# Kernel optimization log

Hardware: AMD Instinct MI355X
Metric: run time of the kernel (lower is better)

Reference implementation:

```python
import jax, jax.numpy as jnp
import numpy as np

DIM = 192
HEADS = 6
WIN = 64  # 8*8
EPS = 1e-12


def setup_inputs() -> dict:
    key = jax.random.key(0)
    ks = jax.random.split(key, 10)
    s = 0.02
    return {
        "qx": jax.random.normal(ks[0], (8192, WIN, DIM), jnp.float32),
        "kvx": jax.random.normal(ks[1], (4096, WIN, DIM), jnp.float32),
        "pos": jax.random.normal(ks[2], (1, WIN, DIM), jnp.float32) * s,
        "Wq": jax.random.normal(ks[3], (DIM, DIM), jnp.float32) * s,
        "bq": jnp.zeros((DIM,), jnp.float32),
        "Wkv": jax.random.normal(ks[4], (2 * DIM, DIM), jnp.float32) * s,
        "bkv": jnp.zeros((2 * DIM,), jnp.float32),
        "Wp": jax.random.normal(ks[5], (DIM, DIM), jnp.float32) * s,
        "bp": jnp.zeros((DIM,), jnp.float32),
    }


def _l2norm(x):
    # F.normalize: x / max(||x||_2, eps) along last dim
    n = jnp.sqrt(jnp.sum(x * x, axis=-1, keepdims=True))
    return x / jnp.maximum(n, EPS)


def reference(qx, kvx, pos, Wq, bq, Wkv, bkv, Wp, bp):
    B_q, q_len, C = qx.shape
    B_kv, kv_len, _ = kvx.shape
    tile_num = B_q // B_kv
    kvx = jnp.tile(kvx, (tile_num, 1, 1))
    qx = qx + pos
    q = qx @ Wq.T + bq                       # [Bq, q, C]
    kv = kvx @ Wkv.T + bkv                   # [Bq, kv, 2C]
    k, v = kv[..., :C], kv[..., C:]
    hd = C // HEADS
    q = q.reshape(B_q, q_len, HEADS, hd).transpose(0, 2, 1, 3)
    k = k.reshape(B_q, kv_len, HEADS, hd).transpose(0, 2, 1, 3)
    v = v.reshape(B_q, kv_len, HEADS, hd).transpose(0, 2, 1, 3)
    scale = 1.0 / np.sqrt(C).astype(np.float32)
    attn = jnp.einsum("bhqd,bhkd->bhqk", _l2norm(q), _l2norm(k)) * scale
    attn = jax.nn.softmax(attn, axis=-1)
    x = jnp.einsum("bhqk,bhkd->bhqd", attn, v)
    x = x.transpose(0, 2, 1, 3).reshape(B_q, q_len, C)
    return x @ Wp.T + bp
```

## Files before the change

kernel.cpp:

```cpp
#include <hip/hip_runtime.h>
#include <hip/hip_bf16.h>

#define TPB   512
#define CDIM  192
#define LDA   200
#define LDST  200
#define SCALE 0.07216878364870323f
#define EPSF  1e-12f

using short8 = __attribute__((ext_vector_type(8))) short;
using f32x4  = __attribute__((ext_vector_type(4))) float;
using us4    = __attribute__((ext_vector_type(4))) unsigned short;

__device__ __forceinline__ unsigned short hc(float f) {
  __hip_bfloat16 h = __float2bfloat16(f);
  unsigned short u; __builtin_memcpy(&u, &h, 2); return u;
}
__device__ __forceinline__ unsigned pack2(float x, float y) {
  return (unsigned)hc(x) | ((unsigned)hc(y) << 16);
}
#define MFMA(a, b, c) __builtin_amdgcn_mfma_f32_16x16x32_bf16((a), (b), (c), 0, 0, 0)
#define SCHED_FENCE() __builtin_amdgcn_sched_barrier(0)

#define NWQ  36864
#define NWKV 73728
#define NWP  36864
__global__ void cvt_weights(const float* __restrict__ Wq, const float* __restrict__ Wkv,
                            const float* __restrict__ Wp, unsigned short* __restrict__ o) {
  int i = blockIdx.x * blockDim.x + threadIdx.x;
  if (i < NWQ) o[i] = hc(Wq[i]);
  else if (i < NWQ + NWKV) o[i] = hc(Wkv[i - NWQ]);
  else if (i < NWQ + NWKV + NWP) o[i] = hc(Wp[i - NWQ - NWKV]);
}

__global__ __launch_bounds__(TPB, 4) void wa_v13(
    const float* __restrict__ qx, const float* __restrict__ kvx,
    const float* __restrict__ pos,
    const float* __restrict__ bq, const float* __restrict__ bkv,
    const float* __restrict__ bp,
    const unsigned short* __restrict__ Wqb, const unsigned short* __restrict__ Wkvb,
    const unsigned short* __restrict__ Wpb,
    float* __restrict__ out, int BQ, int BKV)
{
  __shared__ __align__(16) unsigned short sA[64 * LDA];
  __shared__ __align__(16) unsigned short sU[64 * LDST];

  const int tid = threadIdx.x;
  const int wid = tid >> 6;
  const int l15 = (tid & 63) & 15;
  const int l4  = (tid & 63) >> 4;

  int g = blockIdx.x;
  int w;
  if (BQ == 2 * BKV && (BKV & 7) == 0) {
    w = ((g >> 4) << 3) + (g & 7) + (((g >> 3) & 1) ? BKV : 0);
  } else {
    w = g;
  }
  const size_t qoff  = (size_t)w * (64 * CDIM);
  const size_t kvoff = (size_t)(w % BKV) * (64 * CDIM);

  const int srcA = l15 + 32 * (l4 & 1);
  const int srcB = srcA + 16;
  const int sel  = l4 >> 1;
  auto redistC = [&](f32x4 cA, f32x4 cB) -> short8 {
    unsigned iA0 = pack2(cA[0], cA[1]), iA1 = pack2(cA[2], cA[3]);
    unsigned iB0 = pack2(cB[0], cB[1]), iB1 = pack2(cB[2], cB[3]);
    unsigned A00 = (unsigned)__shfl((int)iA0, srcA);
    unsigned A01 = (unsigned)__shfl((int)iA1, srcA);
    unsigned A10 = (unsigned)__shfl((int)iB0, srcA);
    unsigned A11 = (unsigned)__shfl((int)iB1, srcA);
    unsigned B00 = (unsigned)__shfl((int)iA0, srcB);
    unsigned B01 = (unsigned)__shfl((int)iA1, srcB);
    unsigned B10 = (unsigned)__shfl((int)iB0, srcB);
    unsigned B11 = (unsigned)__shfl((int)iB1, srcB);
    union { uint4 u; short8 s; } uu;
    uu.u.x = sel ? A10 : A00;
    uu.u.y = sel ? A11 : A01;
    uu.u.z = sel ? B10 : B00;
    uu.u.w = sel ? B11 : B01;
    return uu.s;
  };

  {
    const float4* gq = (const float4*)(qx + qoff);
    const float4* p4 = (const float4*)pos;
    #pragma unroll
    for (int t = 0; t < 6; ++t) {
      int e = tid + t * TPB, row = e / 48, c4 = e % 48;
      float4 a = gq[e], p = p4[e];
      us4 wq;
      wq.x = hc(a.x + p.x); wq.y = hc(a.y + p.y); wq.z = hc(a.z + p.z); wq.w = hc(a.w + p.w);
      *(us4*)&sA[row * LDA + c4 * 4] = wq;
    }
    const float4* gk = (const float4*)(kvx + kvoff);
    #pragma unroll
    for (int t = 0; t < 6; ++t) {
      int e = tid + t * TPB, row = e / 48, c4 = e % 48;
      float4 k = gk[e];
      us4 wk; wk.x = hc(k.x); wk.y = hc(k.y); wk.z = hc(k.z); wk.w = hc(k.w);
      *(us4*)&sU[row * LDST + c4 * 4] = wk;
    }
  }
  __syncthreads();

  const int h = wid;

  short8 kres[4];
  short8 av[2][2];
  if (wid < 6) {
    {
      f32x4 kacc[4][2];
      #pragma unroll
      for (int mh = 0; mh < 2; ++mh) {
        float4 bk = *(const float4*)&bkv[32 * h + 16 * mh + 4 * l4];
        #pragma unroll
        for (int n = 0; n < 4; ++n) kacc[n][mh] = f32x4{bk.x, bk.y, bk.z, bk.w};
      }
      #pragma unroll
      for (int ks = 0; ks < 6; ++ks) {
        short8 act[4];
        #pragma unroll
        for (int n = 0; n < 4; ++n)
          act[n] = *(const short8*)&sU[(16 * n + l15) * LDST + ks * 32 + 8 * l4];
        #pragma unroll
        for (int mh = 0; mh < 2; ++mh) {
          short8 kw = *(const short8*)&Wkvb[(size_t)(32 * h + 16 * mh + l15) * CDIM + ks * 32 + 8 * l4];
          #pragma unroll
          for (int n = 0; n < 4; ++n) kacc[n][mh] = MFMA(kw, act[n], kacc[n][mh]);
        }
      }
      #pragma unroll
      for (int n = 0; n < 4; ++n) {
        float ss = 0.f;
        #pragma unroll
        for (int mh = 0; mh < 2; ++mh)
          #pragma unroll
          for (int r = 0; r < 4; ++r) ss += kacc[n][mh][r] * kacc[n][mh][r];
        ss += __shfl_xor(ss, 16);
        ss += __shfl_xor(ss, 32);
        float sc = 1.0f / fmaxf(sqrtf(ss), EPSF);
        #pragma unroll
        for (int mh = 0; mh < 2; ++mh)
          #pragma unroll
          for (int r = 0; r < 4; ++r) kacc[n][mh][r] *= sc;
        kres[n] = redistC(kacc[n][0], kacc[n][1]);
      }
    }
    SCHED_FENCE();
    {
      f32x4 vacc[4][2];
      #pragma unroll
      for (int nv = 0; nv < 2; ++nv) {
        float bv = bkv[CDIM + 32 * h + 16 * nv + l15];
        #pragma unroll
        for (int m = 0; m < 4; ++m) vacc[m][nv] = f32x4{bv, bv, bv, bv};
      }
      #pragma unroll
      for (int ks = 0; ks < 6; ++ks) {
        short8 act[4];
        #pragma unroll
        for (int n = 0; n < 4; ++n)
          act[n] = *(const short8*)&sU[(16 * n + l15) * LDST + ks * 32 + 8 * l4];
        #pragma unroll
        for (int nv = 0; nv < 2; ++nv) {
          short8 vw = *(const short8*)&Wkvb[(size_t)(CDIM + 32 * h + 16 * nv + l15) * CDIM + ks * 32 + 8 * l4];
          #pragma unroll
          for (int m = 0; m < 4; ++m) vacc[m][nv] = MFMA(act[m], vw, vacc[m][nv]);
        }
      }
      #pragma unroll
      for (int cc = 0; cc < 2; ++cc)
        #pragma unroll
        for (int nv = 0; nv < 2; ++nv)
          av[cc][nv] = redistC(vacc[2 * cc][nv], vacc[2 * cc + 1][nv]);
    }
  }
  __syncthreads();

  if (wid < 6) {
    short8 qres[4];
    {
      f32x4 qacc[4][2];
      #pragma unroll
      for (int mh = 0; mh < 2; ++mh) {
        float4 bk = *(const float4*)&bq[32 * h + 16 * mh + 4 * l4];
        #pragma unroll
        for (int n = 0; n < 4; ++n) qacc[n][mh] = f32x4{bk.x, bk.y, bk.z, bk.w};
      }
      #pragma unroll
      for (int ks = 0; ks < 6; ++ks) {
        short8 act[4];
        #pragma unroll
        for (int n = 0; n < 4; ++n)
          act[n] = *(const short8*)&sA[(16 * n + l15) * LDA + ks * 32 + 8 * l4];
        #pragma unroll
        for (int mh = 0; mh < 2; ++mh) {
          short8 qw = *(const short8*)&Wqb[(size_t)(32 * h + 16 * mh + l15) * CDIM + ks * 32 + 8 * l4];
          #pragma unroll
          for (int n = 0; n < 4; ++n) qacc[n][mh] = MFMA(qw, act[n], qacc[n][mh]);
        }
      }
      #pragma unroll
      for (int n = 0; n < 4; ++n) {
        float ss = 0.f;
        #pragma unroll
        for (int mh = 0; mh < 2; ++mh)
          #pragma unroll
          for (int r = 0; r < 4; ++r) ss += qacc[n][mh][r] * qacc[n][mh][r];
        ss += __shfl_xor(ss, 16);
        ss += __shfl_xor(ss, 32);
        float sc = SCALE / fmaxf(sqrtf(ss), EPSF);
        #pragma unroll
        for (int mh = 0; mh < 2; ++mh)
          #pragma unroll
          for (int r = 0; r < 4; ++r) qacc[n][mh][r] *= sc;
        qres[n] = redistC(qacc[n][0], qacc[n][1]);
      }
    }
    SCHED_FENCE();
    #pragma unroll
    for (int t = 0; t < 4; ++t) {
      f32x4 c[4];
      #pragma unroll
      for (int n = 0; n < 4; ++n) {
        f32x4 z = f32x4{0.f, 0.f, 0.f, 0.f};
        c[n] = MFMA(kres[n], qres[t], z);
      }
      float mx = c[0][0];
      #pragma unroll
      for (int n = 0; n < 4; ++n)
        #pragma unroll
        for (int r = 0; r < 4; ++r) mx = fmaxf(mx, c[n][r]);
      mx = fmaxf(mx, __shfl_xor(mx, 16));
      mx = fmaxf(mx, __shfl_xor(mx, 32));
      float sum = 0.f;
      #pragma unroll
      for (int n = 0; n < 4; ++n)
        #pragma unroll
        for (int r = 0; r < 4; ++r) { c[n][r] = __expf(c[n][r] - mx); sum += c[n][r]; }
      sum += __shfl_xor(sum, 16);
      sum += __shfl_xor(sum, 32);
      const float inv = 1.0f / sum;
      #pragma unroll
      for (int n = 0; n < 4; ++n)
        #pragma unroll
        for (int r = 0; r < 4; ++r) c[n][r] *= inv;
      short8 pa0 = redistC(c[0], c[1]);
      short8 pa1 = redistC(c[2], c[3]);
      f32x4 cx0 = f32x4{0.f, 0.f, 0.f, 0.f};
      f32x4 cx1 = f32x4{0.f, 0.f, 0.f, 0.f};
      cx0 = MFMA(av[0][0], pa0, cx0);
      cx0 = MFMA(av[1][0], pa1, cx0);
      cx1 = MFMA(av[0][1], pa0, cx1);
      cx1 = MFMA(av[1][1], pa1, cx1);
      short8 xf = redistC(cx0, cx1);
      *(short8*)&sU[(16 * t + l15) * LDST + h * 32 + 8 * l4] = xf;
    }
  }
  __syncthreads();

  {
    {
      const int n = wid;
      f32x4 oacc[4];
      float bv = bp[n * 16 + l15];
      #pragma unroll
      for (int m = 0; m < 4; ++m) oacc[m] = f32x4{bv, bv, bv, bv};
      #pragma unroll
      for (int ks = 0; ks < 6; ++ks) {
        short8 pw = *(const short8*)&Wpb[(size_t)(n * 16 + l15) * CDIM + ks * 32 + 8 * l4];
        #pragma unroll
        for (int m = 0; m < 4; ++m) {
          short8 xa = *(const short8*)&sU[(16 * m + l15) * LDST + ks * 32 + 8 * l4];
          oacc[m] = MFMA(xa, pw, oacc[m]);
        }
      }
      #pragma unroll
      for (int m = 0; m < 4; ++m)
        #pragma unroll
        for (int r = 0; r < 4; ++r)
          out[qoff + (size_t)(16 * m + 4 * l4 + r) * CDIM + n * 16 + l15] = oacc[m][r];
    }
    SCHED_FENCE();
    if (wid >= 4) {
      const int n = wid + 4;
      f32x4 oacc[4];
      float bv = bp[n * 16 + l15];
      #pragma unroll
      for (int m = 0; m < 4; ++m) oacc[m] = f32x4{bv, bv, bv, bv};
      #pragma unroll
      for (int ks = 0; ks < 6; ++ks) {
        short8 pw = *(const short8*)&Wpb[(size_t)(n * 16 + l15) * CDIM + ks * 32 + 8 * l4];
        #pragma unroll
        for (int m = 0; m < 4; ++m) {
          short8 xa = *(const short8*)&sU[(16 * m + l15) * LDST + ks * 32 + 8 * l4];
          oacc[m] = MFMA(xa, pw, oacc[m]);
        }
      }
      #pragma unroll
      for (int m = 0; m < 4; ++m)
        #pragma unroll
        for (int r = 0; r < 4; ++r)
          out[qoff + (size_t)(16 * m + 4 * l4 + r) * CDIM + n * 16 + l15] = oacc[m][r];
    }
  }
}

extern "C" void kernel_launch(void* const* d_in, const int* in_sizes, int n_in,
                              void* d_out, int out_size, void* d_ws, size_t ws_size,
                              hipStream_t stream) {
  const float* qx  = (const float*)d_in[0];
  const float* kvx = (const float*)d_in[1];
  const float* pos = (const float*)d_in[2];
  const float* Wq  = (const float*)d_in[3];
  const float* bq  = (const float*)d_in[4];
  const float* Wkv = (const float*)d_in[5];
  const float* bkv = (const float*)d_in[6];
  const float* Wp  = (const float*)d_in[7];
  const float* bp  = (const float*)d_in[8];
  float* out = (float*)d_out;
  unsigned short* wsb = (unsigned short*)d_ws;

  const int BQ  = in_sizes[0] / (64 * CDIM);
  const int BKV = in_sizes[1] / (64 * CDIM);

  const int ncvt = NWQ + NWKV + NWP;
  cvt_weights<<<(ncvt + 255) / 256, 256, 0, stream>>>(Wq, Wkv, Wp, wsb);

  wa_v13<<<BQ, TPB, 0, stream>>>(qx, kvx, pos, bq, bkv, bp,
                                 wsb, wsb + NWQ, wsb + NWQ + NWKV, out, BQ, BKV);
}
```

Before: 482.4 us.

## Reuse K/V projections across tiled query windows within one block

The grid now has one block per KV window instead of one per query window. Each block computes the K/V projection and normalization once, then loops over the tile_num query windows that share that KV window. This removes the redundant K/V projection and kvx loading that the old per-query-window blocks repeated. In exchange the grid is halved (4096 blocks), giving less parallelism, and the next Q window is staged only after the output projection, serially, with an extra barrier per iteration.

```diff
diff --git a/kernel.cpp b/kernel.cpp
--- a/kernel.cpp
+++ b/kernel.cpp
@@ -33,14 +33,14 @@
   else if (i < NWQ + NWKV + NWP) o[i] = hc(Wp[i - NWQ - NWKV]);
 }
 
-__global__ __launch_bounds__(TPB, 4) void wa_v13(
+__global__ __launch_bounds__(TPB, 4) void wa_v14(
     const float* __restrict__ qx, const float* __restrict__ kvx,
     const float* __restrict__ pos,
     const float* __restrict__ bq, const float* __restrict__ bkv,
     const float* __restrict__ bp,
     const unsigned short* __restrict__ Wqb, const unsigned short* __restrict__ Wkvb,
     const unsigned short* __restrict__ Wpb,
-    float* __restrict__ out, int BQ, int BKV)
+    float* __restrict__ out, int BKV, int tile_num)
 {
   __shared__ __align__(16) unsigned short sA[64 * LDA];
   __shared__ __align__(16) unsigned short sU[64 * LDST];
@@ -49,16 +49,8 @@
   const int wid = tid >> 6;
   const int l15 = (tid & 63) & 15;
   const int l4  = (tid & 63) >> 4;
-
-  int g = blockIdx.x;
-  int w;
-  if (BQ == 2 * BKV && (BKV & 7) == 0) {
-    w = ((g >> 4) << 3) + (g & 7) + (((g >> 3) & 1) ? BKV : 0);
-  } else {
-    w = g;
-  }
-  const size_t qoff  = (size_t)w * (64 * CDIM);
-  const size_t kvoff = (size_t)(w % BKV) * (64 * CDIM);
+  const int b   = blockIdx.x;
+  const size_t kvoff = (size_t)b * (64 * CDIM);
 
   const int srcA = l15 + 32 * (l4 & 1);
   const int srcB = srcA + 16;
@@ -82,8 +74,8 @@
     return uu.s;
   };
 
-  {
-    const float4* gq = (const float4*)(qx + qoff);
+  auto stage_q = [&](size_t qo) {
+    const float4* gq = (const float4*)(qx + qo);
     const float4* p4 = (const float4*)pos;
     #pragma unroll
     for (int t = 0; t < 6; ++t) {
@@ -93,6 +85,10 @@
       wq.x = hc(a.x + p.x); wq.y = hc(a.y + p.y); wq.z = hc(a.z + p.z); wq.w = hc(a.w + p.w);
       *(us4*)&sA[row * LDA + c4 * 4] = wq;
     }
+  };
+
+  stage_q(kvoff );
+  {
     const float4* gk = (const float4*)(kvx + kvoff);
     #pragma unroll
     for (int t = 0; t < 6; ++t) {
@@ -178,98 +174,100 @@
   }
   __syncthreads();
 
-  if (wid < 6) {
-    short8 qres[4];
+  for (int wq = 0; wq < tile_num; ++wq) {
+    const size_t qoff = kvoff + (size_t)wq * BKV * (64 * CDIM);
+
+    if (wid < 6) {
+      short8 qres[4];
+      {
+        f32x4 qacc[4][2];
+        #pragma unroll
+        for (int mh = 0; mh < 2; ++mh) {
+          float4 bk = *(const float4*)&bq[32 * h + 16 * mh + 4 * l4];
+          #pragma unroll
+          for (int n = 0; n < 4; ++n) qacc[n][mh] = f32x4{bk.x, bk.y, bk.z, bk.w};
+        }
+        #pragma unroll
+        for (int ks = 0; ks < 6; ++ks) {
+          short8 act[4];
+          #pragma unroll
+          for (int n = 0; n < 4; ++n)
+            act[n] = *(const short8*)&sA[(16 * n + l15) * LDA + ks * 32 + 8 * l4];
+          #pragma unroll
+          for (int mh = 0; mh < 2; ++mh) {
+            short8 qw = *(const short8*)&Wqb[(size_t)(32 * h + 16 * mh + l15) * CDIM + ks * 32 + 8 * l4];
+            #pragma unroll
+            for (int n = 0; n < 4; ++n) qacc[n][mh] = MFMA(qw, act[n], qacc[n][mh]);
+          }
+        }
+        #pragma unroll
+        for (int n = 0; n < 4; ++n) {
+          float ss = 0.f;
+          #pragma unroll
+          for (int mh = 0; mh < 2; ++mh)
+            #pragma unroll
+            for (int r = 0; r < 4; ++r) ss += qacc[n][mh][r] * qacc[n][mh][r];
+          ss += __shfl_xor(ss, 16);
+          ss += __shfl_xor(ss, 32);
+          float sc = SCALE / fmaxf(sqrtf(ss), EPSF);
+          #pragma unroll
+          for (int mh = 0; mh < 2; ++mh)
+            #pragma unroll
+            for (int r = 0; r < 4; ++r) qacc[n][mh][r] *= sc;
+          qres[n] = redistC(qacc[n][0], qacc[n][1]);
+        }
+      }
+      SCHED_FENCE();
+      #pragma unroll
+      for (int t = 0; t < 4; ++t) {
+        f32x4 c[4];
+        #pragma unroll
+        for (int n = 0; n < 4; ++n) {
+          f32x4 z = f32x4{0.f, 0.f, 0.f, 0.f};
+          c[n] = MFMA(kres[n], qres[t], z);
+        }
+        float mx = c[0][0];
+        #pragma unroll
+        for (int n = 0; n < 4; ++n)
+          #pragma unroll
+          for (int r = 0; r < 4; ++r) mx = fmaxf(mx, c[n][r]);
+        mx = fmaxf(mx, __shfl_xor(mx, 16));
+        mx = fmaxf(mx, __shfl_xor(mx, 32));
+        float sum = 0.f;
+        #pragma unroll
+        for (int n = 0; n < 4; ++n)
+          #pragma unroll
+          for (int r = 0; r < 4; ++r) { c[n][r] = __expf(c[n][r] - mx); sum += c[n][r]; }
+        sum += __shfl_xor(sum, 16);
+        sum += __shfl_xor(sum, 32);
+        const float inv = 1.0f / sum;
+        #pragma unroll
+        for (int n = 0; n < 4; ++n)
+          #pragma unroll
+          for (int r = 0; r < 4; ++r) c[n][r] *= inv;
+        short8 pa0 = redistC(c[0], c[1]);
+        short8 pa1 = redistC(c[2], c[3]);
+        f32x4 cx0 = f32x4{0.f, 0.f, 0.f, 0.f};
+        f32x4 cx1 = f32x4{0.f, 0.f, 0.f, 0.f};
+        cx0 = MFMA(av[0][0], pa0, cx0);
+        cx0 = MFMA(av[1][0], pa1, cx0);
+        cx1 = MFMA(av[0][1], pa0, cx1);
+        cx1 = MFMA(av[1][1], pa1, cx1);
+        short8 xf = redistC(cx0, cx1);
+        *(short8*)&sU[(16 * t + l15) * LDST + h * 32 + 8 * l4] = xf;
+      }
+    }
+    __syncthreads();
+
     {
-      f32x4 qacc[4][2];
-      #pragma unroll
-      for (int mh = 0; mh < 2; ++mh) {
-        float4 bk = *(const float4*)&bq[32 * h + 16 * mh + 4 * l4];
-        #pragma unroll
-        for (int n = 0; n < 4; ++n) qacc[n][mh] = f32x4{bk.x, bk.y, bk.z, bk.w};
-      }
+      const int n0 = wid;
+      f32x4 oacc[4];
+      float bv = bp[n0 * 16 + l15];
+      #pragma unroll
+      for (int m = 0; m < 4; ++m) oacc[m] = f32x4{bv, bv, bv, bv};
       #pragma unroll
       for (int ks = 0; ks < 6; ++ks) {
-        short8 act[4];
-        #pragma unroll
-        for (int n = 0; n < 4; ++n)
-          act[n] = *(const short8*)&sA[(16 * n + l15) * LDA + ks * 32 + 8 * l4];
-        #pragma unroll
-        for (int mh = 0; mh < 2; ++mh) {
-          short8 qw = *(const short8*)&Wqb[(size_t)(32 * h + 16 * mh + l15) * CDIM + ks * 32 + 8 * l4];
-          #pragma unroll
-          for (int n = 0; n < 4; ++n) qacc[n][mh] = MFMA(qw, act[n], qacc[n][mh]);
-        }
-      }
-      #pragma unroll
-      for (int n = 0; n < 4; ++n) {
-        float ss = 0.f;
-        #pragma unroll
-        for (int mh = 0; mh < 2; ++mh)
-          #pragma unroll
-          for (int r = 0; r < 4; ++r) ss += qacc[n][mh][r] * qacc[n][mh][r];
-        ss += __shfl_xor(ss, 16);
-        ss += __shfl_xor(ss, 32);
-        float sc = SCALE / fmaxf(sqrtf(ss), EPSF);
-        #pragma unroll
-        for (int mh = 0; mh < 2; ++mh)
-          #pragma unroll
-          for (int r = 0; r < 4; ++r) qacc[n][mh][r] *= sc;
-        qres[n] = redistC(qacc[n][0], qacc[n][1]);
-      }
-    }
-    SCHED_FENCE();
-    #pragma unroll
-    for (int t = 0; t < 4; ++t) {
-      f32x4 c[4];
-      #pragma unroll
-      for (int n = 0; n < 4; ++n) {
-        f32x4 z = f32x4{0.f, 0.f, 0.f, 0.f};
-        c[n] = MFMA(kres[n], qres[t], z);
-      }
-      float mx = c[0][0];
-      #pragma unroll
-      for (int n = 0; n < 4; ++n)
-        #pragma unroll
-        for (int r = 0; r < 4; ++r) mx = fmaxf(mx, c[n][r]);
-      mx = fmaxf(mx, __shfl_xor(mx, 16));
-      mx = fmaxf(mx, __shfl_xor(mx, 32));
-      float sum = 0.f;
-      #pragma unroll
-      for (int n = 0; n < 4; ++n)
-        #pragma unroll
-        for (int r = 0; r < 4; ++r) { c[n][r] = __expf(c[n][r] - mx); sum += c[n][r]; }
-      sum += __shfl_xor(sum, 16);
-      sum += __shfl_xor(sum, 32);
-      const float inv = 1.0f / sum;
-      #pragma unroll
-      for (int n = 0; n < 4; ++n)
-        #pragma unroll
-        for (int r = 0; r < 4; ++r) c[n][r] *= inv;
-      short8 pa0 = redistC(c[0], c[1]);
-      short8 pa1 = redistC(c[2], c[3]);
-      f32x4 cx0 = f32x4{0.f, 0.f, 0.f, 0.f};
-      f32x4 cx1 = f32x4{0.f, 0.f, 0.f, 0.f};
-      cx0 = MFMA(av[0][0], pa0, cx0);
-      cx0 = MFMA(av[1][0], pa1, cx0);
-      cx1 = MFMA(av[0][1], pa0, cx1);
-      cx1 = MFMA(av[1][1], pa1, cx1);
-      short8 xf = redistC(cx0, cx1);
-      *(short8*)&sU[(16 * t + l15) * LDST + h * 32 + 8 * l4] = xf;
-    }
-  }
-  __syncthreads();
-
-  {
-    {
-      const int n = wid;
-      f32x4 oacc[4];
-      float bv = bp[n * 16 + l15];
-      #pragma unroll
-      for (int m = 0; m < 4; ++m) oacc[m] = f32x4{bv, bv, bv, bv};
-      #pragma unroll
-      for (int ks = 0; ks < 6; ++ks) {
-        short8 pw = *(const short8*)&Wpb[(size_t)(n * 16 + l15) * CDIM + ks * 32 + 8 * l4];
+        short8 pw = *(const short8*)&Wpb[(size_t)(n0 * 16 + l15) * CDIM + ks * 32 + 8 * l4];
         #pragma unroll
         for (int m = 0; m < 4; ++m) {
           short8 xa = *(const short8*)&sU[(16 * m + l15) * LDST + ks * 32 + 8 * l4];
@@ -280,30 +278,34 @@
       for (int m = 0; m < 4; ++m)
         #pragma unroll
         for (int r = 0; r < 4; ++r)
-          out[qoff + (size_t)(16 * m + 4 * l4 + r) * CDIM + n * 16 + l15] = oacc[m][r];
-    }
-    SCHED_FENCE();
-    if (wid >= 4) {
-      const int n = wid + 4;
-      f32x4 oacc[4];
-      float bv = bp[n * 16 + l15];
-      #pragma unroll
-      for (int m = 0; m < 4; ++m) oacc[m] = f32x4{bv, bv, bv, bv};
-      #pragma unroll
-      for (int ks = 0; ks < 6; ++ks) {
-        short8 pw = *(const short8*)&Wpb[(size_t)(n * 16 + l15) * CDIM + ks * 32 + 8 * l4];
-        #pragma unroll
-        for (int m = 0; m < 4; ++m) {
-          short8 xa = *(const short8*)&sU[(16 * m + l15) * LDST + ks * 32 + 8 * l4];
-          oacc[m] = MFMA(xa, pw, oacc[m]);
-        }
-      }
-      #pragma unroll
-      for (int m = 0; m < 4; ++m)
-        #pragma unroll
-        for (int r = 0; r < 4; ++r)
-          out[qoff + (size_t)(16 * m + 4 * l4 + r) * CDIM + n * 16 + l15] = oacc[m][r];
-    }
+          out[qoff + (size_t)(16 * m + 4 * l4 + r) * CDIM + n0 * 16 + l15] = oacc[m][r];
+
+      SCHED_FENCE();
+      if (wid < 4) {
+        const int n1 = wid + 8;
+        f32x4 oacc2[4];
+        float bv2 = bp[n1 * 16 + l15];
+        #pragma unroll
+        for (int m = 0; m < 4; ++m) oacc2[m] = f32x4{bv2, bv2, bv2, bv2};
+        #pragma unroll
+        for (int ks = 0; ks < 6; ++ks) {
+          short8 pw = *(const short8*)&Wpb[(size_t)(n1 * 16 + l15) * CDIM + ks * 32 + 8 * l4];
+          #pragma unroll
+          for (int m = 0; m < 4; ++m) {
+            short8 xa = *(const short8*)&sU[(16 * m + l15) * LDST + ks * 32 + 8 * l4];
+            oacc2[m] = MFMA(xa, pw, oacc2[m]);
+          }
+        }
+        #pragma unroll
+        for (int m = 0; m < 4; ++m)
+          #pragma unroll
+          for (int r = 0; r < 4; ++r)
+            out[qoff + (size_t)(16 * m + 4 * l4 + r) * CDIM + n1 * 16 + l15] = oacc2[m][r];
+      }
+      if (wq + 1 < tile_num)
+        stage_q(kvoff + (size_t)(wq + 1) * BKV * (64 * CDIM));
+    }
+    __syncthreads();
   }
 }
 
@@ -324,10 +326,11 @@
 
   const int BQ  = in_sizes[0] / (64 * CDIM);
   const int BKV = in_sizes[1] / (64 * CDIM);
+  const int tile_num = BQ / BKV;
 
   const int ncvt = NWQ + NWKV + NWP;
   cvt_weights<<<(ncvt + 255) / 256, 256, 0, stream>>>(Wq, Wkv, Wp, wsb);
 
-  wa_v13<<<BQ, TPB, 0, stream>>>(qx, kvx, pos, bq, bkv, bp,
-                                 wsb, wsb + NWQ, wsb + NWQ + NWKV, out, BQ, BKV);
-}
+  wa_v14<<<BKV, TPB, 0, stream>>>(qx, kvx, pos, bq, bkv, bp,
+                                  wsb, wsb + NWQ, wsb + NWQ + NWKV, out, BKV, tile_num);
+}
```

Measured after the change: 574.7 us. 1.19x slower.
